# Optimization experiments

Hardware: AMD Instinct MI355X
Metric: run time of the kernel (lower is better)

## Reference

```python
import jax, jax.numpy as jnp
import numpy as np

B, V, DIN, DOUT, DEPTH = 128, 512, 511, 256, 8

def setup_inputs() -> dict:
    key = jax.random.key(0)
    k0, k1, k2, k3, k4 = jax.random.split(key, 5)
    return {
        "inp": jax.random.uniform(k0, (B, DIN), jnp.float32) / DIN,
        "visible_units": jax.random.normal(k1, (V, DIN), jnp.float32),
        "L": jax.random.normal(k2, (DEPTH, V), jnp.float32) * 0.1,
        "visible_fs": jax.random.normal(k3, (V, DOUT), jnp.float32),
        "biases": jax.random.normal(k4, (DEPTH, DOUT), jnp.float32) * 0.1,
    }

def reference(inp, visible_units, L, visible_fs, biases):
    b = inp.shape[0]
    f0 = jnp.broadcast_to(visible_fs, (b,) + visible_fs.shape)          # (B,V,DOUT)
    h0 = jnp.broadcast_to(visible_units, (b,) + visible_units.shape)    # (B,V,DIN)
    # first input weights: cat(1 - sum(inp), inp) -> (B, V) since V = DIN+1
    iw0 = jnp.concatenate([1.0 - jnp.sum(inp, axis=1, keepdims=True), inp], axis=1)
    rows = jnp.arange(b)

    def step(carry, xs):
        iw, f, h = carry
        Li, bi = xs
        w = jax.nn.softmax(Li)                      # (V,)  softmax(L[i])
        w_det = jax.lax.stop_gradient(w)            # detached copy used for routing
        div = iw / (w_det + 1e-20)                  # (B,V)
        idx = jnp.argmin(div, axis=1)               # (B,) torch.min indices
        vals = jnp.take_along_axis(div, idx[:, None], axis=1)[:, 0]  # (B,)
        iw_new = iw - vals[:, None] * w_det
        iw_new = iw_new.at[rows, idx].set(vals)
        h_old = h
        new_h = jnp.einsum('v,bvd->bd', w, h)       # (B,DIN)  matmul(weights, h)
        new_f = jnp.einsum('v,bvo->bo', w, f) + bi  # (B,DOUT) matmul(weights, f)+bias
        f = f.at[rows, idx].set(new_f)
        h = h.at[rows, idx].set(new_h)
        return (iw_new, f, h), (h_old, new_h)

    (iw, f, h), (h_old_stack, sel_stack) = jax.lax.scan(step, (iw0, f0, h0), (L, biases))
    out = jnp.einsum('bv,bvo->bo', iw, f)[:, None, :]   # (B,1,DOUT)
    last_h = sel_stack[-1]                               # (B,DIN)
    return out, h_old_stack, sel_stack, last_h
```

## Files before the change

kernel.cpp:

```cpp
#include <hip/hip_runtime.h>
#include <cstddef>

#define B_   128
#define V_   512
#define DIN_ 511
#define DOUT_ 256
#define DEPTH_ 8

__global__ void k_softmax(const float* __restrict__ L, float* __restrict__ W) {
    const int i = blockIdx.x;
    const int t = threadIdx.x;
    __shared__ float red[256];
    float x0 = L[i * V_ + t];
    float x1 = L[i * V_ + 256 + t];
    float m = fmaxf(x0, x1);
    red[t] = m; __syncthreads();
    for (int s = 128; s > 0; s >>= 1) {
        if (t < s) red[t] = fmaxf(red[t], red[t + s]);
        __syncthreads();
    }
    const float mx = red[0];
    __syncthreads();
    float e0 = expf(x0 - mx), e1 = expf(x1 - mx);
    red[t] = e0 + e1; __syncthreads();
    for (int s = 128; s > 0; s >>= 1) {
        if (t < s) red[t] += red[t + s];
        __syncthreads();
    }
    const float inv = 1.0f / red[0];
    W[i * V_ + t]       = e0 * inv;
    W[i * V_ + 256 + t] = e1 * inv;
}

__global__ void k_base(const float* __restrict__ W, const float* __restrict__ vu,
                       const float* __restrict__ vfs,
                       float* __restrict__ baseH, float* __restrict__ baseF) {
    const int bx = blockIdx.x;
    const int i = bx / 3, part = bx % 3;
    const int t = threadIdx.x;
    __shared__ float Wl[V_];
    Wl[t] = W[i * V_ + t];
    Wl[t + 256] = W[i * V_ + 256 + t];
    __syncthreads();
    if (part < 2) {
        int d = part * 256 + t;
        if (d < DIN_) {
            float acc = 0.0f;
            for (int v = 0; v < V_; ++v) acc += Wl[v] * vu[v * DIN_ + d];
            baseH[i * DIN_ + d] = acc;
        }
    } else {
        int o = t;
        float acc = 0.0f;
        for (int v = 0; v < V_; ++v) acc += Wl[v] * vfs[v * DOUT_ + o];
        baseF[i * DOUT_ + o] = acc;
    }
}

__global__ void __launch_bounds__(256)
k_scan(const float* __restrict__ inp, const float* __restrict__ vu,
       const float* __restrict__ vfs, const float* __restrict__ biases,
       const float* __restrict__ W, const float* __restrict__ baseH,
       const float* __restrict__ baseF,
       float* __restrict__ out, float* __restrict__ sel, float* __restrict__ lasth,
       int* __restrict__ idxh_g) {
    const int b = blockIdx.x;
    const int t = threadIdx.x;

    __shared__ float iw[V_];
    __shared__ float Wl[V_];
    __shared__ float selh[DEPTH_][DIN_];
    __shared__ float fvals[DEPTH_][DOUT_];
    __shared__ float redv[256];
    __shared__ int   redi[256];
    __shared__ int   idxh[DEPTH_];

    float x0 = inp[b * DIN_ + t];
    float x1 = (t < 255) ? inp[b * DIN_ + 256 + t] : 0.0f;
    redv[t] = x0 + x1; __syncthreads();
    for (int s = 128; s > 0; s >>= 1) {
        if (t < s) redv[t] += redv[t + s];
        __syncthreads();
    }
    if (t == 0) iw[0] = 1.0f - redv[0];
    iw[t + 1] = x0;
    if (t < 255) iw[t + 257] = x1;
    __syncthreads();

    for (int i = 0; i < DEPTH_; ++i) {
        Wl[t] = W[i * V_ + t];
        Wl[t + 256] = W[i * V_ + 256 + t];
        __syncthreads();

        float d0 = iw[t]       / (Wl[t]       + 1e-20f);
        float d1 = iw[t + 256] / (Wl[t + 256] + 1e-20f);
        float bv; int bi;
        if (d0 <= d1) { bv = d0; bi = t; } else { bv = d1; bi = t + 256; }
        redv[t] = bv; redi[t] = bi; __syncthreads();
        for (int s = 128; s > 0; s >>= 1) {
            if (t < s) {
                float ov = redv[t + s]; int oi = redi[t + s];
                if (ov < redv[t] || (ov == redv[t] && oi < redi[t])) {
                    redv[t] = ov; redi[t] = oi;
                }
            }
            __syncthreads();
        }
        const float mval = redv[0];
        const int   midx = redi[0];
        __syncthreads();

        iw[t]       -= mval * Wl[t];
        iw[t + 256] -= mval * Wl[t + 256];
        __syncthreads();
        if (t == 0) { iw[midx] = mval; idxh[i] = midx; }
        __syncthreads();

        for (int d = t; d < DIN_; d += 256) {
            float acc = baseH[i * DIN_ + d];
            for (int j = 0; j < i; ++j) {
                int r = idxh[j];
                bool alive = true;
                for (int j2 = j + 1; j2 < i; ++j2)
                    if (idxh[j2] == r) { alive = false; break; }
                if (alive) acc += Wl[r] * (selh[j][d] - vu[r * DIN_ + d]);
            }
            selh[i][d] = acc;
            sel[(size_t)(i * B_ + b) * DIN_ + d] = acc;
        }
        {
            int o = t;
            float acc = baseF[i * DOUT_ + o] + biases[i * DOUT_ + o];
            for (int j = 0; j < i; ++j) {
                int r = idxh[j];
                bool alive = true;
                for (int j2 = j + 1; j2 < i; ++j2)
                    if (idxh[j2] == r) { alive = false; break; }
                if (alive) acc += Wl[r] * (fvals[j][o] - vfs[r * DOUT_ + o]);
            }
            fvals[i][o] = acc;
        }
        __syncthreads();
    }

    {
        int o = t;
        float acc = 0.0f;
        for (int v = 0; v < V_; ++v) acc += iw[v] * vfs[v * DOUT_ + o];
        for (int j = 0; j < DEPTH_; ++j) {
            int r = idxh[j];
            bool alive = true;
            for (int j2 = j + 1; j2 < DEPTH_; ++j2)
                if (idxh[j2] == r) { alive = false; break; }
            if (alive) acc += iw[r] * (fvals[j][o] - vfs[r * DOUT_ + o]);
        }
        out[b * DOUT_ + o] = acc;
    }
    for (int d = t; d < DIN_; d += 256)
        lasth[b * DIN_ + d] = selh[DEPTH_ - 1][d];
    if (t < DEPTH_) idxh_g[b * DEPTH_ + t] = idxh[t];
}

__global__ void k_planes(const float* __restrict__ vu, float* __restrict__ hold) {
    const int CH = 4;
    const int F4_PER_PLANE = (V_ * DIN_) / 4;
    const int F4_PER_CHUNK = F4_PER_PLANE / CH;
    const int bx = blockIdx.x;
    const int p = bx / CH, c = bx % CH;
    const float4* __restrict__ src = (const float4*)vu;
    float4* __restrict__ dst = (float4*)hold + (size_t)p * F4_PER_PLANE;
    const int end = (c + 1) * F4_PER_CHUNK;
    for (int k = c * F4_PER_CHUNK + threadIdx.x; k < end; k += 256)
        dst[k] = src[k];
}

__global__ void k_fixrows(const float* __restrict__ sel, const int* __restrict__ idxh_g,
                          float* __restrict__ hold) {
    const int p = blockIdx.x;
    const int i = p >> 7;
    const int b = p & 127;
    const int t = threadIdx.x;
    for (int j = 0; j < i; ++j) {
        int r = idxh_g[b * DEPTH_ + j];
        bool alive = true;
        for (int j2 = j + 1; j2 < i; ++j2)
            if (idxh_g[b * DEPTH_ + j2] == r) { alive = false; break; }
        if (!alive) continue;
        const float* __restrict__ src = sel + (size_t)(j * B_ + b) * DIN_;
        float* __restrict__ dst = hold + ((size_t)p * V_ + r) * DIN_;
        for (int d = t; d < DIN_; d += 128) dst[d] = src[d];
    }
}

extern "C" void kernel_launch(void* const* d_in, const int* in_sizes, int n_in,
                              void* d_out, int out_size, void* d_ws, size_t ws_size,
                              hipStream_t stream) {
    const float* inp    = (const float*)d_in[0];
    const float* vu     = (const float*)d_in[1];
    const float* L      = (const float*)d_in[2];
    const float* vfs    = (const float*)d_in[3];
    const float* biases = (const float*)d_in[4];

    float* out   = (float*)d_out;
    float* hold  = out + (size_t)B_ * DOUT_;
    float* sel   = hold + (size_t)DEPTH_ * B_ * V_ * DIN_;
    float* lasth = sel + (size_t)DEPTH_ * B_ * DIN_;

    float* W     = (float*)d_ws;
    float* baseH = W + DEPTH_ * V_;
    float* baseF = baseH + DEPTH_ * DIN_;
    int*   idxh  = (int*)(baseF + DEPTH_ * DOUT_);

    k_softmax<<<DEPTH_, 256, 0, stream>>>(L, W);
    k_base<<<DEPTH_ * 3, 256, 0, stream>>>(W, vu, vfs, baseH, baseF);
    k_scan<<<B_, 256, 0, stream>>>(inp, vu, vfs, biases, W, baseH, baseF,
                                   out, sel, lasth, idxh);
    k_planes<<<DEPTH_ * B_ * 4, 256, 0, stream>>>(vu, hold);
    k_fixrows<<<DEPTH_ * B_, 128, 0, stream>>>(sel, idxh, hold);
}
```

Baseline: 1.167 ms.

## Fuse softmax into base kernel, merge plane copy into scan launch, use wave shuffles

Softmax is folded into the base-projection kernel, so each block recomputes the weights and only one block per depth writes them. The large plane-broadcast copy now runs as extra blocks of the scan kernel, so the copy overlaps the serial per-batch scan instead of following it. Copy stores are nontemporal, and shared-memory tree reductions are replaced by wavefront shuffle reductions. This removes a few launches and syncs, but mixes two very different workloads in one grid, where the copy blocks can compete with the scan blocks for bandwidth and CU slots.

Result: faster. 1.103 ms (-5.5%).

```diff
diff --git a/kernel.cpp b/kernel.cpp
--- a/kernel.cpp
+++ b/kernel.cpp
@@ -1,120 +1,151 @@
 #include <hip/hip_runtime.h>
 #include <cstddef>
 
-#define B_   128
-#define V_   512
-#define DIN_ 511
+#define B_    128
+#define V_    512
+#define DIN_  511
 #define DOUT_ 256
 #define DEPTH_ 8
 
-__global__ void k_softmax(const float* __restrict__ L, float* __restrict__ W) {
-    const int i = blockIdx.x;
-    const int t = threadIdx.x;
-    __shared__ float red[256];
-    float x0 = L[i * V_ + t];
-    float x1 = L[i * V_ + 256 + t];
-    float m = fmaxf(x0, x1);
-    red[t] = m; __syncthreads();
-    for (int s = 128; s > 0; s >>= 1) {
-        if (t < s) red[t] = fmaxf(red[t], red[t + s]);
-        __syncthreads();
-    }
-    const float mx = red[0];
-    __syncthreads();
-    float e0 = expf(x0 - mx), e1 = expf(x1 - mx);
-    red[t] = e0 + e1; __syncthreads();
-    for (int s = 128; s > 0; s >>= 1) {
-        if (t < s) red[t] += red[t + s];
-        __syncthreads();
-    }
-    const float inv = 1.0f / red[0];
-    W[i * V_ + t]       = e0 * inv;
-    W[i * V_ + 256 + t] = e1 * inv;
-}
-
-__global__ void k_base(const float* __restrict__ W, const float* __restrict__ vu,
-                       const float* __restrict__ vfs,
-                       float* __restrict__ baseH, float* __restrict__ baseF) {
+typedef float f32x4 __attribute__((ext_vector_type(4)));
+
+__global__ void __launch_bounds__(256)
+k_prep(const float* __restrict__ L, const float* __restrict__ vu,
+       const float* __restrict__ vfs,
+       float* __restrict__ W, float* __restrict__ baseH, float* __restrict__ baseF) {
     const int bx = blockIdx.x;
     const int i = bx / 3, part = bx % 3;
     const int t = threadIdx.x;
+    const int lane = t & 63, wid = t >> 6;
     __shared__ float Wl[V_];
-    Wl[t] = W[i * V_ + t];
-    Wl[t + 256] = W[i * V_ + 256 + t];
-    __syncthreads();
-    if (part < 2) {
+    __shared__ float red[4];
+
+    float x0 = L[i * V_ + t];
+    float x1 = L[i * V_ + 256 + t];
+
+    float m = fmaxf(x0, x1);
+    #pragma unroll
+    for (int off = 32; off; off >>= 1) m = fmaxf(m, __shfl_xor(m, off, 64));
+    if (lane == 0) red[wid] = m;
+    __syncthreads();
+    const float mx = fmaxf(fmaxf(red[0], red[1]), fmaxf(red[2], red[3]));
+
+    float e0 = expf(x0 - mx), e1 = expf(x1 - mx);
+    float s = e0 + e1;
+    #pragma unroll
+    for (int off = 32; off; off >>= 1) s += __shfl_xor(s, off, 64);
+    __syncthreads();
+    if (lane == 0) red[wid] = s;
+    __syncthreads();
+    const float inv = 1.0f / (red[0] + red[1] + red[2] + red[3]);
+
+    Wl[t] = e0 * inv;
+    Wl[t + 256] = e1 * inv;
+    __syncthreads();
+
+    if (part == 2) {
+        W[i * V_ + t] = Wl[t];
+        W[i * V_ + 256 + t] = Wl[t + 256];
+        float acc = 0.0f;
+        for (int v = 0; v < V_; ++v) acc += Wl[v] * vfs[v * DOUT_ + t];
+        baseF[i * DOUT_ + t] = acc;
+    } else {
         int d = part * 256 + t;
         if (d < DIN_) {
             float acc = 0.0f;
             for (int v = 0; v < V_; ++v) acc += Wl[v] * vu[v * DIN_ + d];
             baseH[i * DIN_ + d] = acc;
         }
-    } else {
-        int o = t;
-        float acc = 0.0f;
-        for (int v = 0; v < V_; ++v) acc += Wl[v] * vfs[v * DOUT_ + o];
-        baseF[i * DOUT_ + o] = acc;
     }
 }
 
 __global__ void __launch_bounds__(256)
-k_scan(const float* __restrict__ inp, const float* __restrict__ vu,
+k_main(const float* __restrict__ inp, const float* __restrict__ vu,
        const float* __restrict__ vfs, const float* __restrict__ biases,
        const float* __restrict__ W, const float* __restrict__ baseH,
        const float* __restrict__ baseF,
-       float* __restrict__ out, float* __restrict__ sel, float* __restrict__ lasth,
-       int* __restrict__ idxh_g) {
+       float* __restrict__ out, float* __restrict__ sel,
+       float* __restrict__ lasth, int* __restrict__ idxh_g,
+       float* __restrict__ hold) {
+    const int t = threadIdx.x;
+
+    if (blockIdx.x >= B_) {
+        const int cb = blockIdx.x - B_;
+        const int CH = 4;
+        const int F4_PER_PLANE = (V_ * DIN_) / 4;
+        const int F4_PER_CHUNK = F4_PER_PLANE / CH;
+        const int p = cb / CH, c = cb % CH;
+        const f32x4* __restrict__ src = (const f32x4*)vu;
+        f32x4* __restrict__ dst = (f32x4*)hold + (size_t)p * F4_PER_PLANE;
+        const int end = (c + 1) * F4_PER_CHUNK;
+        #pragma unroll 4
+        for (int k = c * F4_PER_CHUNK + t; k < end; k += 256) {
+            f32x4 v = src[k];
+            __builtin_nontemporal_store(v, &dst[k]);
+        }
+        return;
+    }
+
     const int b = blockIdx.x;
-    const int t = threadIdx.x;
+    const int lane = t & 63, wid = t >> 6;
 
     __shared__ float iw[V_];
     __shared__ float Wl[V_];
     __shared__ float selh[DEPTH_][DIN_];
     __shared__ float fvals[DEPTH_][DOUT_];
-    __shared__ float redv[256];
-    __shared__ int   redi[256];
+    __shared__ float redf[4];
+    __shared__ int   redi[4];
+    __shared__ float bcv;
+    __shared__ int   bci;
     __shared__ int   idxh[DEPTH_];
 
     float x0 = inp[b * DIN_ + t];
     float x1 = (t < 255) ? inp[b * DIN_ + 256 + t] : 0.0f;
-    redv[t] = x0 + x1; __syncthreads();
-    for (int s = 128; s > 0; s >>= 1) {
-        if (t < s) redv[t] += redv[t + s];
-        __syncthreads();
-    }
-    if (t == 0) iw[0] = 1.0f - redv[0];
+    float ssum = x0 + x1;
+    #pragma unroll
+    for (int off = 32; off; off >>= 1) ssum += __shfl_xor(ssum, off, 64);
+    if (lane == 0) redf[wid] = ssum;
     iw[t + 1] = x0;
     if (t < 255) iw[t + 257] = x1;
+    __syncthreads();
+    if (t == 0) iw[0] = 1.0f - (redf[0] + redf[1] + redf[2] + redf[3]);
     __syncthreads();
 
     for (int i = 0; i < DEPTH_; ++i) {
         Wl[t] = W[i * V_ + t];
         Wl[t + 256] = W[i * V_ + 256 + t];
         __syncthreads();
-
-        float d0 = iw[t]       / (Wl[t]       + 1e-20f);
-        float d1 = iw[t + 256] / (Wl[t + 256] + 1e-20f);
+        const float w0 = Wl[t], w1 = Wl[t + 256];
+
+        float d0 = iw[t]       / (w0 + 1e-20f);
+        float d1 = iw[t + 256] / (w1 + 1e-20f);
         float bv; int bi;
         if (d0 <= d1) { bv = d0; bi = t; } else { bv = d1; bi = t + 256; }
-        redv[t] = bv; redi[t] = bi; __syncthreads();
-        for (int s = 128; s > 0; s >>= 1) {
-            if (t < s) {
-                float ov = redv[t + s]; int oi = redi[t + s];
-                if (ov < redv[t] || (ov == redv[t] && oi < redi[t])) {
-                    redv[t] = ov; redi[t] = oi;
-                }
+        #pragma unroll
+        for (int off = 32; off; off >>= 1) {
+            float ov = __shfl_xor(bv, off, 64);
+            int   oi = __shfl_xor(bi, off, 64);
+            if (ov < bv || (ov == bv && oi < bi)) { bv = ov; bi = oi; }
+        }
+        if (lane == 0) { redf[wid] = bv; redi[wid] = bi; }
+        __syncthreads();
+        if (t == 0) {
+            float mv = redf[0]; int mi = redi[0];
+            #pragma unroll
+            for (int w = 1; w < 4; ++w) {
+                float ov = redf[w]; int oi = redi[w];
+                if (ov < mv || (ov == mv && oi < mi)) { mv = ov; mi = oi; }
             }
-            __syncthreads();
-        }
-        const float mval = redv[0];
-        const int   midx = redi[0];
-        __syncthreads();
-
-        iw[t]       -= mval * Wl[t];
-        iw[t + 256] -= mval * Wl[t + 256];
-        __syncthreads();
-        if (t == 0) { iw[midx] = mval; idxh[i] = midx; }
-        __syncthreads();
+            bcv = mv; bci = mi; idxh[i] = mi;
+        }
+        __syncthreads();
+        const float mval = bcv;
+        const int   midx = bci;
+
+        iw[t]       -= mval * w0;
+        iw[t + 256] -= mval * w1;
+        __syncthreads();
+        if (t == 0) iw[midx] = mval;
 
         for (int d = t; d < DIN_; d += 256) {
             float acc = baseH[i * DIN_ + d];
@@ -129,53 +160,41 @@
             sel[(size_t)(i * B_ + b) * DIN_ + d] = acc;
         }
         {
-            int o = t;
-            float acc = baseF[i * DOUT_ + o] + biases[i * DOUT_ + o];
+            float acc = baseF[i * DOUT_ + t] + biases[i * DOUT_ + t];
             for (int j = 0; j < i; ++j) {
                 int r = idxh[j];
                 bool alive = true;
                 for (int j2 = j + 1; j2 < i; ++j2)
                     if (idxh[j2] == r) { alive = false; break; }
-                if (alive) acc += Wl[r] * (fvals[j][o] - vfs[r * DOUT_ + o]);
+                if (alive) acc += Wl[r] * (fvals[j][t] - vfs[r * DOUT_ + t]);
             }
-            fvals[i][o] = acc;
+            fvals[i][t] = acc;
         }
         __syncthreads();
     }
 
     {
-        int o = t;
         float acc = 0.0f;
-        for (int v = 0; v < V_; ++v) acc += iw[v] * vfs[v * DOUT_ + o];
+        #pragma unroll 8
+        for (int v = 0; v < V_; ++v) acc += iw[v] * vfs[v * DOUT_ + t];
+        #pragma unroll
         for (int j = 0; j < DEPTH_; ++j) {
             int r = idxh[j];
             bool alive = true;
             for (int j2 = j + 1; j2 < DEPTH_; ++j2)
                 if (idxh[j2] == r) { alive = false; break; }
-            if (alive) acc += iw[r] * (fvals[j][o] - vfs[r * DOUT_ + o]);
-        }
-        out[b * DOUT_ + o] = acc;
+            if (alive) acc += iw[r] * (fvals[j][t] - vfs[r * DOUT_ + t]);
+        }
+        out[b * DOUT_ + t] = acc;
     }
     for (int d = t; d < DIN_; d += 256)
         lasth[b * DIN_ + d] = selh[DEPTH_ - 1][d];
     if (t < DEPTH_) idxh_g[b * DEPTH_ + t] = idxh[t];
 }
 
-__global__ void k_planes(const float* __restrict__ vu, float* __restrict__ hold) {
-    const int CH = 4;
-    const int F4_PER_PLANE = (V_ * DIN_) / 4;
-    const int F4_PER_CHUNK = F4_PER_PLANE / CH;
-    const int bx = blockIdx.x;
-    const int p = bx / CH, c = bx % CH;
-    const float4* __restrict__ src = (const float4*)vu;
-    float4* __restrict__ dst = (float4*)hold + (size_t)p * F4_PER_PLANE;
-    const int end = (c + 1) * F4_PER_CHUNK;
-    for (int k = c * F4_PER_CHUNK + threadIdx.x; k < end; k += 256)
-        dst[k] = src[k];
-}
-
-__global__ void k_fixrows(const float* __restrict__ sel, const int* __restrict__ idxh_g,
-                          float* __restrict__ hold) {
+__global__ void __launch_bounds__(128)
+k_fixrows(const float* __restrict__ sel, const int* __restrict__ idxh_g,
+          float* __restrict__ hold) {
     const int p = blockIdx.x;
     const int i = p >> 7;
     const int b = p & 127;
@@ -211,10 +230,9 @@
     float* baseF = baseH + DEPTH_ * DIN_;
     int*   idxh  = (int*)(baseF + DEPTH_ * DOUT_);
 
-    k_softmax<<<DEPTH_, 256, 0, stream>>>(L, W);
-    k_base<<<DEPTH_ * 3, 256, 0, stream>>>(W, vu, vfs, baseH, baseF);
-    k_scan<<<B_, 256, 0, stream>>>(inp, vu, vfs, biases, W, baseH, baseF,
-                                   out, sel, lasth, idxh);
-    k_planes<<<DEPTH_ * B_ * 4, 256, 0, stream>>>(vu, hold);
+    k_prep<<<DEPTH_ * 3, 256, 0, stream>>>(L, vu, vfs, W, baseH, baseF);
+    k_main<<<B_ + DEPTH_ * B_ * 4, 256, 0, stream>>>(inp, vu, vfs, biases,
+                                                     W, baseH, baseF,
+                                                     out, sel, lasth, idxh, hold);
     k_fixrows<<<DEPTH_ * B_, 128, 0, stream>>>(sel, idxh, hold);
 }
```
